# Performance work log

Hardware: AMD Instinct MI355X
Metric: run time of the kernel (lower is better)

## Reference

```python
import jax, jax.numpy as jnp
import numpy as np

B_SZ, L_SEQ, D_MODEL, D_STATE = 4, 2048, 1024, 16


def setup_inputs() -> dict:
    key = jax.random.key(0)
    ks = jax.random.split(key, 6)
    x = jax.random.normal(ks[0], (B_SZ, L_SEQ, D_MODEL), jnp.float32)
    # HiPPO-inspired init: A_log = log(arange(1..n)).clamp(min=-7), broadcast over channels
    A_log = jnp.clip(jnp.log(jnp.arange(1, D_STATE + 1, dtype=jnp.float32)), -7.0, None)
    A_log = jnp.broadcast_to(A_log[None, :], (D_MODEL, D_STATE)).astype(jnp.float32)
    B_param = 0.02 * jax.random.normal(ks[1], (D_MODEL, D_STATE), jnp.float32)
    C_param = 0.02 * jax.random.normal(ks[2], (D_MODEL, D_STATE), jnp.float32)
    log_dt = 0.01 * jax.random.normal(ks[3], (D_MODEL,), jnp.float32) - 4.0
    in_w = jax.random.normal(ks[4], (2 * D_MODEL, D_MODEL), jnp.float32) / np.sqrt(D_MODEL).astype(np.float32)
    in_b = jnp.zeros((2 * D_MODEL,), jnp.float32)
    out_w = jax.random.normal(ks[5], (D_MODEL, D_MODEL), jnp.float32) / np.sqrt(D_MODEL).astype(np.float32)
    out_b = jnp.zeros((D_MODEL,), jnp.float32)
    ln_g = jnp.ones((D_MODEL,), jnp.float32)
    ln_b = jnp.zeros((D_MODEL,), jnp.float32)
    return {"x": x, "A_log": A_log, "B_param": B_param, "C_param": C_param,
            "log_dt": log_dt, "in_w": in_w, "in_b": in_b, "out_w": out_w,
            "out_b": out_b, "ln_g": ln_g, "ln_b": ln_b}


def _ssm_scan(u, A_log, B_param, C_param, log_dt):
    # u: (B, L, D). Builds kernel h[t,d] = sum_n A_bar[d,n]^t * C[d,n]*B[d,n]*dt[d]
    # and applies a causal depthwise convolution (via FFT; same math as conv1d).
    L = u.shape[1]
    dt = jnp.clip(jnp.exp(log_dt), 1e-4, 1.0)                      # (D,)
    A_bar = jnp.exp(-jnp.exp(A_log) * dt[:, None])                 # ZOH discretisation (D,N)
    A_bar = jnp.clip(A_bar, 1e-8, 1.0 - 1e-8)
    log_A = jnp.log(A_bar)                                         # (D,N)
    t_idx = jnp.arange(L, dtype=jnp.float32)                       # (L,)
    A_powers = jnp.exp(t_idx[:, None, None] * log_A[None, :, :])   # (L,D,N)
    cb_dt = C_param * B_param * dt[:, None]                        # (D,N)
    kernel = jnp.einsum('ldn,dn->ld', A_powers, cb_dt)             # (L,D)
    # causal conv: y[b,t,d] = sum_{tau<=t} kernel[tau,d] * u[b,t-tau,d]
    n_fft = 2 * L
    Kf = jnp.fft.rfft(kernel, n=n_fft, axis=0)                     # (n_fft/2+1, D)
    Uf = jnp.fft.rfft(u, n=n_fft, axis=1)                          # (B, n_fft/2+1, D)
    y = jnp.fft.irfft(Uf * Kf[None], n=n_fft, axis=1)[:, :L]       # (B,L,D)
    return y.astype(u.dtype)


def reference(x, A_log, B_param, C_param, log_dt, in_w, in_b, out_w, out_b, ln_g, ln_b):
    x = x.astype(jnp.float32)
    residual = x
    # LayerNorm (eps=1e-5)
    mu = jnp.mean(x, axis=-1, keepdims=True)
    var = jnp.mean(jnp.square(x - mu), axis=-1, keepdims=True)
    xn = (x - mu) * jax.lax.rsqrt(var + 1e-5) * ln_g + ln_b
    xz = xn @ in_w.T + in_b                                        # (B,L,2D)
    x_proj, z = xz[..., :D_MODEL], xz[..., D_MODEL:]
    z = jax.nn.silu(z)
    y = _ssm_scan(x_proj, A_log, B_param, C_param, log_dt)
    y = y * z
    y = y @ out_w.T + out_b
    # dropout is identity in eval mode
    return jnp.clip(y + residual, -10.0, 10.0)
```

## Files before the change

### kernel.cpp

```cpp
#include <hip/hip_runtime.h>
#include <hip/hip_bf16.h>

#define D_MODEL 1024
#define D_STATE 16
#define L_SEQ 2048
#define B_SZ 4
#define M_ROWS (B_SZ * L_SEQ)
#define N_CHUNK 32
#define C_LEN 64

typedef __attribute__((ext_vector_type(8))) short short8;
typedef __attribute__((ext_vector_type(4))) float f32x4;
typedef unsigned int u32;
typedef __attribute__((ext_vector_type(4))) u32 u32x4;

static __device__ __forceinline__ unsigned short f2bf(float f) {
    unsigned int u = __float_as_uint(f);
    unsigned int r = (u + 0x7FFFu + ((u >> 16) & 1u)) >> 16;
    return (unsigned short)r;
}
static __device__ __forceinline__ float bf2f(unsigned short u) {
    return __uint_as_float(((unsigned int)u) << 16);
}

__global__ void conv_bf16_kernel(const float* __restrict__ src,
                                 unsigned short* __restrict__ dst, int n4) {
    int i = blockIdx.x * blockDim.x + threadIdx.x;
    if (i < n4) {
        float4 v = ((const float4*)src)[i];
        ushort4 o;
        o.x = f2bf(v.x); o.y = f2bf(v.y); o.z = f2bf(v.z); o.w = f2bf(v.w);
        ((ushort4*)dst)[i] = o;
    }
}

__global__ __launch_bounds__(256) void ln_kernel(const float* __restrict__ x,
                                                 const float* __restrict__ g,
                                                 const float* __restrict__ b,
                                                 unsigned short* __restrict__ xn) {
    int row = blockIdx.x;
    int t = threadIdx.x;
    const float4* xr = (const float4*)(x + (size_t)row * D_MODEL);
    float4 v = xr[t];
    float s  = v.x + v.y + v.z + v.w;
    float ss = v.x * v.x + v.y * v.y + v.z * v.z + v.w * v.w;
    #pragma unroll
    for (int o = 32; o > 0; o >>= 1) {
        s  += __shfl_down(s,  o);
        ss += __shfl_down(ss, o);
    }
    __shared__ float sbuf[8];
    int wid = t >> 6;
    if ((t & 63) == 0) { sbuf[wid] = s; sbuf[4 + wid] = ss; }
    __syncthreads();
    float S  = sbuf[0] + sbuf[1] + sbuf[2] + sbuf[3];
    float SS = sbuf[4] + sbuf[5] + sbuf[6] + sbuf[7];
    float mu  = S * (1.0f / D_MODEL);
    float var = SS * (1.0f / D_MODEL) - mu * mu;
    float inv = rsqrtf(var + 1e-5f);
    float4 gv = ((const float4*)g)[t];
    float4 bv = ((const float4*)b)[t];
    ushort4 o;
    o.x = f2bf((v.x - mu) * inv * gv.x + bv.x);
    o.y = f2bf((v.y - mu) * inv * gv.y + bv.y);
    o.z = f2bf((v.z - mu) * inv * gv.z + bv.z);
    o.w = f2bf((v.w - mu) * inv * gv.w + bv.w);
    ((ushort4*)(xn + (size_t)row * D_MODEL))[t] = o;
}

__global__ __launch_bounds__(256, 2) void gemm1_kernel(const unsigned short* __restrict__ A,
                                                       const unsigned short* __restrict__ Bt,
                                                       const float* __restrict__ bias,
                                                       unsigned short* __restrict__ u_bf,
                                                       unsigned short* __restrict__ zs) {
    __shared__ unsigned short lA[2][128 * 32];
    __shared__ unsigned short lB[2][256 * 32];
    const int K = D_MODEL;

    int t = threadIdx.x;
    int lane = t & 63;
    int wave = t >> 6;
    int wm = wave >> 1, wn = wave & 1;
    int m0 = blockIdx.y * 128;
    int n0 = blockIdx.x * 256;
    int row = lane & 15;
    int quad = lane >> 4;

    int sr = t >> 2;
    int sc = ((t & 3) ^ ((t >> 3) & 3)) * 8;
    const unsigned short* gA0 = A + (size_t)(m0 + sr) * K + sc;
    const unsigned short* gA1 = A + (size_t)(m0 + 64 + sr) * K + sc;
    const unsigned short* gB0 = Bt + (size_t)(n0 + sr) * K + sc;
    const unsigned short* gB1 = Bt + (size_t)(n0 + 64 + sr) * K + sc;
    const unsigned short* gB2 = Bt + (size_t)(n0 + 128 + sr) * K + sc;
    const unsigned short* gB3 = Bt + (size_t)(n0 + 192 + sr) * K + sc;

    int offA[4], offB[8];
    #pragma unroll
    for (int i = 0; i < 4; i++) {
        int r6 = i * 16 + row;
        int slot = r6 * 4 + (quad ^ ((r6 >> 1) & 3));
        offA[i] = wm * 2048 + slot * 8;
    }
    #pragma unroll
    for (int j = 0; j < 8; j++) {
        int r8 = wn * 128 + j * 16 + row;
        int half = r8 >> 6, r6 = r8 & 63;
        int slot = r6 * 4 + (quad ^ ((r6 >> 1) & 3));
        offB[j] = half * 2048 + slot * 8;
    }

    u32x4 pa0 = *(const u32x4*)gA0;
    u32x4 pa1 = *(const u32x4*)gA1;
    u32x4 pb0 = *(const u32x4*)gB0;
    u32x4 pb1 = *(const u32x4*)gB1;
    u32x4 pb2 = *(const u32x4*)gB2;
    u32x4 pb3 = *(const u32x4*)gB3;

    f32x4 acc[4][8] = {};

    for (int kk = 0; kk < K; kk += 32) {
        int buf = (kk >> 5) & 1;
        unsigned short* sA = lA[buf];
        unsigned short* sB = lB[buf];
        *(u32x4*)&sA[t * 8]        = pa0;
        *(u32x4*)&sA[2048 + t * 8] = pa1;
        *(u32x4*)&sB[t * 8]        = pb0;
        *(u32x4*)&sB[2048 + t * 8] = pb1;
        *(u32x4*)&sB[4096 + t * 8] = pb2;
        *(u32x4*)&sB[6144 + t * 8] = pb3;
        __syncthreads();
        int kn = kk + 32;
        if (kn < K) {
            pa0 = *(const u32x4*)(gA0 + kn);
            pa1 = *(const u32x4*)(gA1 + kn);
            pb0 = *(const u32x4*)(gB0 + kn);
            pb1 = *(const u32x4*)(gB1 + kn);
            pb2 = *(const u32x4*)(gB2 + kn);
            pb3 = *(const u32x4*)(gB3 + kn);
        }
        short8 a[4];
        #pragma unroll
        for (int i = 0; i < 4; i++) a[i] = *(const short8*)&sA[offA[i]];
        #pragma unroll
        for (int j = 0; j < 8; j++) {
            short8 b = *(const short8*)&sB[offB[j]];
            #pragma unroll
            for (int i = 0; i < 4; i++)
                acc[i][j] = __builtin_amdgcn_mfma_f32_16x16x32_bf16(a[i], b, acc[i][j], 0, 0, 0);
        }
    }

    int col = row;
    #pragma unroll
    for (int j = 0; j < 8; j++) {
        int n = n0 + wn * 128 + j * 16 + col;
        float bs = bias[n];
        #pragma unroll
        for (int i = 0; i < 4; i++) {
            #pragma unroll
            for (int r = 0; r < 4; r++) {
                int m = m0 + wm * 64 + i * 16 + quad * 4 + r;
                float v = acc[i][j][r] + bs;
                if (n < D_MODEL) {
                    u_bf[(size_t)m * D_MODEL + n] = f2bf(v);
                } else {
                    float sv = v / (1.0f + __expf(-v));
                    zs[(size_t)m * D_MODEL + (n - D_MODEL)] = f2bf(sv);
                }
            }
        }
    }
}

__global__ __launch_bounds__(256) void gemm2_kernel(const unsigned short* __restrict__ A,
                                                    const unsigned short* __restrict__ Bt,
                                                    const float* __restrict__ bias,
                                                    float* __restrict__ out_f,
                                                    const float* __restrict__ resid) {
    __shared__ unsigned short lA[2][128 * 32];
    __shared__ unsigned short lB[2][128 * 32];
    const int K = D_MODEL;

    int t = threadIdx.x;
    int lane = t & 63;
    int wave = t >> 6;
    int wm = wave >> 1, wn = wave & 1;
    int m0 = blockIdx.y * 128;
    int n0 = blockIdx.x * 128;
    int row = lane & 15;
    int quad = lane >> 4;

    int sr = t >> 2;
    int sc = ((t & 3) ^ ((t >> 3) & 3)) * 8;
    const unsigned short* gA0 = A + (size_t)(m0 + sr) * K + sc;
    const unsigned short* gA1 = A + (size_t)(m0 + 64 + sr) * K + sc;
    const unsigned short* gB0 = Bt + (size_t)(n0 + sr) * K + sc;
    const unsigned short* gB1 = Bt + (size_t)(n0 + 64 + sr) * K + sc;

    int offA[4], offB[4];
    #pragma unroll
    for (int i = 0; i < 4; i++) {
        int r6 = i * 16 + row;
        int slot = r6 * 4 + (quad ^ ((r6 >> 1) & 3));
        offA[i] = wm * 2048 + slot * 8;
        offB[i] = wn * 2048 + slot * 8;
    }

    u32x4 pa0 = *(const u32x4*)gA0;
    u32x4 pa1 = *(const u32x4*)gA1;
    u32x4 pb0 = *(const u32x4*)gB0;
    u32x4 pb1 = *(const u32x4*)gB1;

    f32x4 acc[4][4] = {};

    for (int kk = 0; kk < K; kk += 32) {
        int buf = (kk >> 5) & 1;
        unsigned short* sA = lA[buf];
        unsigned short* sB = lB[buf];
        *(u32x4*)&sA[t * 8]        = pa0;
        *(u32x4*)&sA[2048 + t * 8] = pa1;
        *(u32x4*)&sB[t * 8]        = pb0;
        *(u32x4*)&sB[2048 + t * 8] = pb1;
        __syncthreads();
        int kn = kk + 32;
        if (kn < K) {
            pa0 = *(const u32x4*)(gA0 + kn);
            pa1 = *(const u32x4*)(gA1 + kn);
            pb0 = *(const u32x4*)(gB0 + kn);
            pb1 = *(const u32x4*)(gB1 + kn);
        }
        short8 a[4], b[4];
        #pragma unroll
        for (int i = 0; i < 4; i++) a[i] = *(const short8*)&sA[offA[i]];
        #pragma unroll
        for (int j = 0; j < 4; j++) b[j] = *(const short8*)&sB[offB[j]];
        #pragma unroll
        for (int i = 0; i < 4; i++)
            #pragma unroll
            for (int j = 0; j < 4; j++)
                acc[i][j] = __builtin_amdgcn_mfma_f32_16x16x32_bf16(a[i], b[j], acc[i][j], 0, 0, 0);
    }

    int col = row;
    #pragma unroll
    for (int i = 0; i < 4; i++) {
        #pragma unroll
        for (int j = 0; j < 4; j++) {
            int n = n0 + wn * 64 + j * 16 + col;
            float bs = bias[n];
            #pragma unroll
            for (int r = 0; r < 4; r++) {
                int m = m0 + wm * 64 + i * 16 + quad * 4 + r;
                float y = acc[i][j][r] + bs + resid[(size_t)m * D_MODEL + n];
                y = fminf(10.0f, fmaxf(-10.0f, y));
                out_f[(size_t)m * D_MODEL + n] = y;
            }
        }
    }
}

static __device__ __forceinline__ void load_params(const float* __restrict__ A_log,
                                                   const float* __restrict__ log_dt,
                                                   int d, float* ab, float& dt_out) {
    float dt = fminf(1.0f, fmaxf(1e-4f, __expf(log_dt[d])));
    #pragma unroll
    for (int n = 0; n < D_STATE; n++) {
        float a = __expf(-__expf(A_log[d * D_STATE + n]) * dt);
        ab[n] = fminf(1.0f - 1e-8f, fmaxf(1e-8f, a));
    }
    dt_out = dt;
}

__global__ __launch_bounds__(256) void scan1_kernel(const unsigned short* __restrict__ u,
                                                    const float* __restrict__ A_log,
                                                    const float* __restrict__ log_dt,
                                                    float* __restrict__ s_local) {
    int gid = blockIdx.x * 256 + threadIdx.x;
    int d = gid & (D_MODEL - 1);
    int c = (gid >> 10) & (N_CHUNK - 1);
    int b = gid >> 15;

    float ab[D_STATE], dt;
    load_params(A_log, log_dt, d, ab, dt);

    float s[D_STATE];
    #pragma unroll
    for (int n = 0; n < D_STATE; n++) s[n] = 0.0f;

    const unsigned short* up = u + ((size_t)(b * L_SEQ + c * C_LEN)) * D_MODEL + d;
    for (int t = 0; t < C_LEN; t++) {
        float uv = bf2f(up[(size_t)t * D_MODEL]);
        #pragma unroll
        for (int n = 0; n < D_STATE; n++) s[n] = fmaf(ab[n], s[n], uv);
    }
    float* sl = s_local + ((size_t)(b * N_CHUNK + c) * D_STATE) * D_MODEL + d;
    #pragma unroll
    for (int n = 0; n < D_STATE; n++) sl[(size_t)n * D_MODEL] = s[n];
}

__global__ __launch_bounds__(256) void scan_combine_kernel(const float* __restrict__ s_local,
                                                           const float* __restrict__ A_log,
                                                           const float* __restrict__ log_dt,
                                                           float* __restrict__ s_init) {
    int gid = blockIdx.x * 256 + threadIdx.x;
    int d = gid & (D_MODEL - 1);
    int n = (gid >> 10) & (D_STATE - 1);
    int b = gid >> 14;

    float dt = fminf(1.0f, fmaxf(1e-4f, __expf(log_dt[d])));
    float a = __expf(-__expf(A_log[d * D_STATE + n]) * dt);
    a = fminf(1.0f - 1e-8f, fmaxf(1e-8f, a));
    float aP = a;
    #pragma unroll
    for (int q = 0; q < 6; q++) aP = aP * aP;

    float s = 0.0f;
    size_t stride_c = (size_t)D_STATE * D_MODEL;
    const float* sl = s_local + ((size_t)b * N_CHUNK * D_STATE + n) * D_MODEL + d;
    float* si = s_init + ((size_t)b * N_CHUNK * D_STATE + n) * D_MODEL + d;
    si[0] = 0.0f;
    for (int c = 1; c < N_CHUNK; c++) {
        s = fmaf(aP, s, sl[(size_t)(c - 1) * stride_c]);
        si[(size_t)c * stride_c] = s;
    }
}

__global__ __launch_bounds__(256) void scan2_kernel(const unsigned short* __restrict__ u,
                                                    const unsigned short* __restrict__ zs,
                                                    const float* __restrict__ A_log,
                                                    const float* __restrict__ Bp,
                                                    const float* __restrict__ Cp,
                                                    const float* __restrict__ log_dt,
                                                    const float* __restrict__ s_init,
                                                    unsigned short* __restrict__ yz) {
    int gid = blockIdx.x * 256 + threadIdx.x;
    int d = gid & (D_MODEL - 1);
    int c = (gid >> 10) & (N_CHUNK - 1);
    int b = gid >> 15;

    float ab[D_STATE], dt;
    load_params(A_log, log_dt, d, ab, dt);
    float cb[D_STATE];
    #pragma unroll
    for (int n = 0; n < D_STATE; n++)
        cb[n] = Cp[d * D_STATE + n] * Bp[d * D_STATE + n] * dt;

    float s[D_STATE];
    const float* si = s_init + ((size_t)(b * N_CHUNK + c) * D_STATE) * D_MODEL + d;
    #pragma unroll
    for (int n = 0; n < D_STATE; n++) s[n] = si[(size_t)n * D_MODEL];

    size_t m0 = (size_t)(b * L_SEQ + c * C_LEN);
    const unsigned short* up = u + m0 * D_MODEL + d;
    const unsigned short* zp = zs + m0 * D_MODEL + d;
    unsigned short* yp = yz + m0 * D_MODEL + d;

    for (int t = 0; t < C_LEN; t++) {
        float uv = bf2f(up[(size_t)t * D_MODEL]);
        #pragma unroll
        for (int n = 0; n < D_STATE; n++) s[n] = fmaf(ab[n], s[n], uv);
        float y = 0.0f;
        #pragma unroll
        for (int n = 0; n < D_STATE; n++) y = fmaf(cb[n], s[n], y);
        float zv = bf2f(zp[(size_t)t * D_MODEL]);
        yp[(size_t)t * D_MODEL] = f2bf(y * zv);
    }
}

extern "C" void kernel_launch(void* const* d_in, const int* in_sizes, int n_in,
                              void* d_out, int out_size, void* d_ws, size_t ws_size,
                              hipStream_t stream) {
    const float* x       = (const float*)d_in[0];
    const float* A_log   = (const float*)d_in[1];
    const float* B_param = (const float*)d_in[2];
    const float* C_param = (const float*)d_in[3];
    const float* log_dt  = (const float*)d_in[4];
    const float* in_w    = (const float*)d_in[5];
    const float* in_b    = (const float*)d_in[6];
    const float* out_w   = (const float*)d_in[7];
    const float* out_b   = (const float*)d_in[8];
    const float* ln_g    = (const float*)d_in[9];
    const float* ln_b    = (const float*)d_in[10];
    float* out = (float*)d_out;

    char* ws = (char*)d_ws;
    size_t off = 0;
    unsigned short* xn = (unsigned short*)(ws + off); off += (size_t)M_ROWS * D_MODEL * 2;
    unsigned short* w1 = (unsigned short*)(ws + off); off += (size_t)2 * D_MODEL * D_MODEL * 2;
    unsigned short* u  = (unsigned short*)(ws + off); off += (size_t)M_ROWS * D_MODEL * 2;
    unsigned short* zs = (unsigned short*)(ws + off); off += (size_t)M_ROWS * D_MODEL * 2;
    unsigned short* yz = (unsigned short*)(ws + off); off += (size_t)M_ROWS * D_MODEL * 2;
    unsigned short* w2 = (unsigned short*)(ws + off); off += (size_t)D_MODEL * D_MODEL * 2;
    float* s_local = (float*)(ws + off); off += (size_t)B_SZ * N_CHUNK * D_STATE * D_MODEL * 4;
    float* s_init  = (float*)(ws + off); off += (size_t)B_SZ * N_CHUNK * D_STATE * D_MODEL * 4;

    {
        int n4 = 2 * D_MODEL * D_MODEL / 4;
        conv_bf16_kernel<<<(n4 + 255) / 256, 256, 0, stream>>>(in_w, w1, n4);
    }
    {
        int n4 = D_MODEL * D_MODEL / 4;
        conv_bf16_kernel<<<(n4 + 255) / 256, 256, 0, stream>>>(out_w, w2, n4);
    }

    ln_kernel<<<M_ROWS, 256, 0, stream>>>(x, ln_g, ln_b, xn);

    gemm1_kernel<<<dim3(2 * D_MODEL / 256, M_ROWS / 128), 256, 0, stream>>>(
        xn, w1, in_b, u, zs);

    scan1_kernel<<<(B_SZ * N_CHUNK * D_MODEL) / 256, 256, 0, stream>>>(u, A_log, log_dt, s_local);
    scan_combine_kernel<<<(B_SZ * D_STATE * D_MODEL) / 256, 256, 0, stream>>>(s_local, A_log, log_dt, s_init);
    scan2_kernel<<<(B_SZ * N_CHUNK * D_MODEL) / 256, 256, 0, stream>>>(
        u, zs, A_log, B_param, C_param, log_dt, s_init, yz);

    gemm2_kernel<<<dim3(D_MODEL / 128, M_ROWS / 128), 256, 0, stream>>>(
        yz, w2, out_b, out, x);
}
```

Baseline: 222.1 us.

## Load GEMM A fragments directly from global into registers, swap grid order

Both GEMM kernels stop staging the A (activation) tile through shared memory. Each lane now loads its MFMA A fragment straight from global memory, one k-step ahead in registers, while B keeps its double-buffered LDS path. A custom barrier (waitcnt lgkmcnt plus s_barrier) replaces __syncthreads, and the grid is transposed so blockIdx.x walks M tiles. This cuts LDS traffic and frees shared memory, at the cost of uncoalesced 16-byte strided global loads for A and duplicate A reads across waves sharing wm.

New measurement: 237.9 us. +7.1%, slower.

```diff
diff --git a/kernel.cpp b/kernel.cpp
--- a/kernel.cpp
+++ b/kernel.cpp
@@ -13,6 +13,8 @@
 typedef __attribute__((ext_vector_type(4))) float f32x4;
 typedef unsigned int u32;
 typedef __attribute__((ext_vector_type(4))) u32 u32x4;
+
+#define BAR() asm volatile("s_waitcnt lgkmcnt(0)\n\ts_barrier" ::: "memory")
 
 static __device__ __forceinline__ unsigned short f2bf(float f) {
     unsigned int u = __float_as_uint(f);
@@ -73,7 +75,6 @@
                                                        const float* __restrict__ bias,
                                                        unsigned short* __restrict__ u_bf,
                                                        unsigned short* __restrict__ zs) {
-    __shared__ unsigned short lA[2][128 * 32];
     __shared__ unsigned short lB[2][256 * 32];
     const int K = D_MODEL;
 
@@ -81,27 +82,24 @@
     int lane = t & 63;
     int wave = t >> 6;
     int wm = wave >> 1, wn = wave & 1;
-    int m0 = blockIdx.y * 128;
-    int n0 = blockIdx.x * 256;
+    int m0 = blockIdx.x * 128;
+    int n0 = blockIdx.y * 256;
     int row = lane & 15;
     int quad = lane >> 4;
 
     int sr = t >> 2;
     int sc = ((t & 3) ^ ((t >> 3) & 3)) * 8;
-    const unsigned short* gA0 = A + (size_t)(m0 + sr) * K + sc;
-    const unsigned short* gA1 = A + (size_t)(m0 + 64 + sr) * K + sc;
     const unsigned short* gB0 = Bt + (size_t)(n0 + sr) * K + sc;
     const unsigned short* gB1 = Bt + (size_t)(n0 + 64 + sr) * K + sc;
     const unsigned short* gB2 = Bt + (size_t)(n0 + 128 + sr) * K + sc;
     const unsigned short* gB3 = Bt + (size_t)(n0 + 192 + sr) * K + sc;
 
-    int offA[4], offB[8];
-    #pragma unroll
-    for (int i = 0; i < 4; i++) {
-        int r6 = i * 16 + row;
-        int slot = r6 * 4 + (quad ^ ((r6 >> 1) & 3));
-        offA[i] = wm * 2048 + slot * 8;
-    }
+    const unsigned short* gA[4];
+    #pragma unroll
+    for (int i = 0; i < 4; i++)
+        gA[i] = A + (size_t)(m0 + wm * 64 + i * 16 + row) * K + quad * 8;
+
+    int offB[8];
     #pragma unroll
     for (int j = 0; j < 8; j++) {
         int r8 = wn * 128 + j * 16 + row;
@@ -110,45 +108,42 @@
         offB[j] = half * 2048 + slot * 8;
     }
 
-    u32x4 pa0 = *(const u32x4*)gA0;
-    u32x4 pa1 = *(const u32x4*)gA1;
-    u32x4 pb0 = *(const u32x4*)gB0;
-    u32x4 pb1 = *(const u32x4*)gB1;
-    u32x4 pb2 = *(const u32x4*)gB2;
-    u32x4 pb3 = *(const u32x4*)gB3;
-
     f32x4 acc[4][8] = {};
 
+    u32x4 PB[4];
+    PB[0] = *(const u32x4*)gB0;
+    PB[1] = *(const u32x4*)gB1;
+    PB[2] = *(const u32x4*)gB2;
+    PB[3] = *(const u32x4*)gB3;
+    short8 a_cur[4], a_nxt[4];
+    #pragma unroll
+    for (int i = 0; i < 4; i++) a_cur[i] = *(const short8*)gA[i];
+
     for (int kk = 0; kk < K; kk += 32) {
-        int buf = (kk >> 5) & 1;
-        unsigned short* sA = lA[buf];
-        unsigned short* sB = lB[buf];
-        *(u32x4*)&sA[t * 8]        = pa0;
-        *(u32x4*)&sA[2048 + t * 8] = pa1;
-        *(u32x4*)&sB[t * 8]        = pb0;
-        *(u32x4*)&sB[2048 + t * 8] = pb1;
-        *(u32x4*)&sB[4096 + t * 8] = pb2;
-        *(u32x4*)&sB[6144 + t * 8] = pb3;
-        __syncthreads();
+        unsigned short* sB = lB[(kk >> 5) & 1];
+        *(u32x4*)&sB[t * 8]        = PB[0];
+        *(u32x4*)&sB[2048 + t * 8] = PB[1];
+        *(u32x4*)&sB[4096 + t * 8] = PB[2];
+        *(u32x4*)&sB[6144 + t * 8] = PB[3];
         int kn = kk + 32;
         if (kn < K) {
-            pa0 = *(const u32x4*)(gA0 + kn);
-            pa1 = *(const u32x4*)(gA1 + kn);
-            pb0 = *(const u32x4*)(gB0 + kn);
-            pb1 = *(const u32x4*)(gB1 + kn);
-            pb2 = *(const u32x4*)(gB2 + kn);
-            pb3 = *(const u32x4*)(gB3 + kn);
-        }
-        short8 a[4];
-        #pragma unroll
-        for (int i = 0; i < 4; i++) a[i] = *(const short8*)&sA[offA[i]];
+            PB[0] = *(const u32x4*)(gB0 + kn);
+            PB[1] = *(const u32x4*)(gB1 + kn);
+            PB[2] = *(const u32x4*)(gB2 + kn);
+            PB[3] = *(const u32x4*)(gB3 + kn);
+            #pragma unroll
+            for (int i = 0; i < 4; i++) a_nxt[i] = *(const short8*)(gA[i] + kn);
+        }
+        BAR();
         #pragma unroll
         for (int j = 0; j < 8; j++) {
             short8 b = *(const short8*)&sB[offB[j]];
             #pragma unroll
             for (int i = 0; i < 4; i++)
-                acc[i][j] = __builtin_amdgcn_mfma_f32_16x16x32_bf16(a[i], b, acc[i][j], 0, 0, 0);
-        }
+                acc[i][j] = __builtin_amdgcn_mfma_f32_16x16x32_bf16(a_cur[i], b, acc[i][j], 0, 0, 0);
+        }
+        #pragma unroll
+        for (int i = 0; i < 4; i++) a_cur[i] = a_nxt[i];
     }
 
     int col = row;
@@ -178,7 +173,6 @@
                                                     const float* __restrict__ bias,
                                                     float* __restrict__ out_f,
                                                     const float* __restrict__ resid) {
-    __shared__ unsigned short lA[2][128 * 32];
     __shared__ unsigned short lB[2][128 * 32];
     const int K = D_MODEL;
 
@@ -186,60 +180,60 @@
     int lane = t & 63;
     int wave = t >> 6;
     int wm = wave >> 1, wn = wave & 1;
-    int m0 = blockIdx.y * 128;
-    int n0 = blockIdx.x * 128;
+    int m0 = blockIdx.x * 128;
+    int n0 = blockIdx.y * 128;
     int row = lane & 15;
     int quad = lane >> 4;
 
     int sr = t >> 2;
     int sc = ((t & 3) ^ ((t >> 3) & 3)) * 8;
-    const unsigned short* gA0 = A + (size_t)(m0 + sr) * K + sc;
-    const unsigned short* gA1 = A + (size_t)(m0 + 64 + sr) * K + sc;
     const unsigned short* gB0 = Bt + (size_t)(n0 + sr) * K + sc;
     const unsigned short* gB1 = Bt + (size_t)(n0 + 64 + sr) * K + sc;
 
-    int offA[4], offB[4];
-    #pragma unroll
-    for (int i = 0; i < 4; i++) {
-        int r6 = i * 16 + row;
-        int slot = r6 * 4 + (quad ^ ((r6 >> 1) & 3));
-        offA[i] = wm * 2048 + slot * 8;
-        offB[i] = wn * 2048 + slot * 8;
-    }
-
-    u32x4 pa0 = *(const u32x4*)gA0;
-    u32x4 pa1 = *(const u32x4*)gA1;
-    u32x4 pb0 = *(const u32x4*)gB0;
-    u32x4 pb1 = *(const u32x4*)gB1;
+    const unsigned short* gA[4];
+    #pragma unroll
+    for (int i = 0; i < 4; i++)
+        gA[i] = A + (size_t)(m0 + wm * 64 + i * 16 + row) * K + quad * 8;
+
+    int offB[4];
+    #pragma unroll
+    for (int j = 0; j < 4; j++) {
+        int r6 = wn * 64 + j * 16 + row;
+        int half = r6 >> 6, rr = r6 & 63;
+        int slot = rr * 4 + (quad ^ ((rr >> 1) & 3));
+        offB[j] = half * 2048 + slot * 8;
+    }
 
     f32x4 acc[4][4] = {};
 
+    u32x4 PB[2];
+    PB[0] = *(const u32x4*)gB0;
+    PB[1] = *(const u32x4*)gB1;
+    short8 a_cur[4], a_nxt[4];
+    #pragma unroll
+    for (int i = 0; i < 4; i++) a_cur[i] = *(const short8*)gA[i];
+
     for (int kk = 0; kk < K; kk += 32) {
-        int buf = (kk >> 5) & 1;
-        unsigned short* sA = lA[buf];
-        unsigned short* sB = lB[buf];
-        *(u32x4*)&sA[t * 8]        = pa0;
-        *(u32x4*)&sA[2048 + t * 8] = pa1;
-        *(u32x4*)&sB[t * 8]        = pb0;
-        *(u32x4*)&sB[2048 + t * 8] = pb1;
-        __syncthreads();
+        unsigned short* sB = lB[(kk >> 5) & 1];
+        *(u32x4*)&sB[t * 8]        = PB[0];
+        *(u32x4*)&sB[2048 + t * 8] = PB[1];
         int kn = kk + 32;
         if (kn < K) {
-            pa0 = *(const u32x4*)(gA0 + kn);
-            pa1 = *(const u32x4*)(gA1 + kn);
-            pb0 = *(const u32x4*)(gB0 + kn);
-            pb1 = *(const u32x4*)(gB1 + kn);
-        }
-        short8 a[4], b[4];
-        #pragma unroll
-        for (int i = 0; i < 4; i++) a[i] = *(const short8*)&sA[offA[i]];
-        #pragma unroll
-        for (int j = 0; j < 4; j++) b[j] = *(const short8*)&sB[offB[j]];
-        #pragma unroll
-        for (int i = 0; i < 4; i++)
-            #pragma unroll
-            for (int j = 0; j < 4; j++)
-                acc[i][j] = __builtin_amdgcn_mfma_f32_16x16x32_bf16(a[i], b[j], acc[i][j], 0, 0, 0);
+            PB[0] = *(const u32x4*)(gB0 + kn);
+            PB[1] = *(const u32x4*)(gB1 + kn);
+            #pragma unroll
+            for (int i = 0; i < 4; i++) a_nxt[i] = *(const short8*)(gA[i] + kn);
+        }
+        BAR();
+        #pragma unroll
+        for (int j = 0; j < 4; j++) {
+            short8 b = *(const short8*)&sB[offB[j]];
+            #pragma unroll
+            for (int i = 0; i < 4; i++)
+                acc[i][j] = __builtin_amdgcn_mfma_f32_16x16x32_bf16(a_cur[i], b, acc[i][j], 0, 0, 0);
+        }
+        #pragma unroll
+        for (int i = 0; i < 4; i++) a_cur[i] = a_nxt[i];
     }
 
     int col = row;
@@ -406,7 +400,7 @@
 
     ln_kernel<<<M_ROWS, 256, 0, stream>>>(x, ln_g, ln_b, xn);
 
-    gemm1_kernel<<<dim3(2 * D_MODEL / 256, M_ROWS / 128), 256, 0, stream>>>(
+    gemm1_kernel<<<dim3(M_ROWS / 128, 2 * D_MODEL / 256), 256, 0, stream>>>(
         xn, w1, in_b, u, zs);
 
     scan1_kernel<<<(B_SZ * N_CHUNK * D_MODEL) / 256, 256, 0, stream>>>(u, A_log, log_dt, s_local);
@@ -414,6 +408,6 @@
     scan2_kernel<<<(B_SZ * N_CHUNK * D_MODEL) / 256, 256, 0, stream>>>(
         u, zs, A_log, B_param, C_param, log_dt, s_init, yz);
 
-    gemm2_kernel<<<dim3(D_MODEL / 128, M_ROWS / 128), 256, 0, stream>>>(
+    gemm2_kernel<<<dim3(M_ROWS / 128, D_MODEL / 128), 256, 0, stream>>>(
         yz, w2, out_b, out, x);
 }
```
